# Kernel optimization log

Measured on AMD Instinct MI355X. Metric: run time of the kernel, lower is better.

## Reference

```python
import jax, jax.numpy as jnp
import numpy as np

B, L, E, H = 4, 1024, 1024, 16
D = E // H  # head_dim = 64
K = 3       # conv kernel size
PROB = 0.9  # Bernoulli keep probability


def setup_inputs() -> dict:
    key = jax.random.key(0)
    ks = jax.random.split(key, 8)
    query = jax.random.normal(ks[0], (B, L, E), dtype=jnp.float32)
    keys = jax.random.normal(ks[1], (B, L, E), dtype=jnp.float32)
    values = jax.random.normal(ks[2], (B, L, E), dtype=jnp.float32)
    padding_mask = jax.random.randint(ks[3], (B, L), 0, 2, dtype=jnp.int32)
    causal_mask = jax.random.randint(ks[4], (B, L), 0, 2, dtype=jnp.int32)
    bern_mask = jax.random.bernoulli(ks[5], PROB, (B, H, L)).astype(jnp.int32)
    # learned params: grouped conv (one in/out channel per head) and value linear
    conv_w = jax.random.normal(ks[6], (H, 1, K, K), dtype=jnp.float32) * 0.1
    conv_b = jnp.zeros((H,), dtype=jnp.float32)
    Wv = jax.random.normal(ks[7], (D, D), dtype=jnp.float32) / np.sqrt(D)
    return {"query": query, "keys": keys, "values": values,
            "padding_mask": padding_mask, "causal_mask": causal_mask,
            "bern_mask": bern_mask, "conv_w": conv_w, "conv_b": conv_b, "Wv": Wv}


def _split_heads(x):  # [b, l, (h d)] -> [b, h, l, d]
    b, l, _ = x.shape
    return x.reshape(b, l, H, D).transpose(0, 2, 1, 3)


def reference(query, keys, values, padding_mask, causal_mask, bern_mask, conv_w, conv_b, Wv):
    # queries: grouped conv2d over [b, h=channels, l, d], shape-preserving
    q = _split_heads(query)
    q = jax.lax.conv_general_dilated(
        q, conv_w, window_strides=(1, 1), padding=((1, 1), (1, 1)),
        dimension_numbers=("NCHW", "OIHW", "NCHW"), feature_group_count=H)
    q = q + conv_b[None, :, None, None]
    # keys: Bernoulli-masked fill with -inf, softmax over the SEQ dim (dim=-2)
    k = _split_heads(keys)
    k = jnp.where(bern_mask[..., None].astype(bool), k, -jnp.inf)
    k = jax.nn.softmax(k, axis=-2)
    # values: per-head linear (torch Linear: x @ W^T)
    v = jnp.einsum("bhld,ed->bhle", _split_heads(values), Wv)
    # attention
    energy = jnp.einsum("bhqd,bhkd->bhqk", q, k)
    mask = (padding_mask.astype(bool) & causal_mask.astype(bool))  # [b, k]
    energy = jnp.where(mask[:, None, None, :], jnp.float32(-1e20), energy)
    attn = jax.nn.softmax(energy / jnp.sqrt(jnp.float32(E)), axis=-1)
    out = jnp.einsum("bhqk,bhkd->bhqd", attn, v)
    return out.transpose(0, 2, 1, 3).reshape(query.shape[0], query.shape[1], E)
```

## Files before the change

kernel.cpp:

```cpp
#include <hip/hip_runtime.h>
#include <hip/hip_bf16.h>
#include <math.h>

#define BB 4
#define LL 1024
#define EE 1024
#define HH 16
#define DD 64
#define NCH 8
#define CHROWS 128
#define K2C 0.04508422002777998f
#define BIASC 7.2134752044448f

typedef __attribute__((ext_vector_type(8))) short short8;
typedef __attribute__((ext_vector_type(16))) float f32x16;
typedef __attribute__((ext_vector_type(4))) int int4v;

static __device__ __forceinline__ unsigned short bfbits(float x) {
    __hip_bfloat16 h = __float2bfloat16(x);
    return *(unsigned short*)&h;
}

#define CVTPK(dst, lo_, hi_) \
    asm("v_cvt_pk_bf16_f32 %0, %1, %2" : "=v"(dst) : "v"(lo_), "v"(hi_))
#define PLSWAP(x_, y_) \
    asm("v_permlane32_swap_b32 %0, %1" : "+v"(x_), "+v"(y_))

__global__ __launch_bounds__(256) void prep_kernel(
    const float* __restrict__ query,
    const float* __restrict__ conv_w,
    const float* __restrict__ conv_b,
    const float* __restrict__ values,
    const float* __restrict__ Wv,
    const float* __restrict__ keys,
    const int* __restrict__ bern,
    const int* __restrict__ pad,
    const int* __restrict__ cau,
    __hip_bfloat16* __restrict__ qcb,
    __hip_bfloat16* __restrict__ vt,
    float* __restrict__ pmax,
    float* __restrict__ psum,
    float* __restrict__ maskf) {
    __shared__ __align__(16) char SM[34048];
    int tid = threadIdx.x;
    int bid = blockIdx.x;

    if (bid < 4096) {
        int d = tid & 63;
        int lr = tid >> 6;
        int l0 = (bid & (LL / 4 - 1)) << 2;
        int bh = bid >> 8;
        int h = bh & (HH - 1);
        int b = bh >> 4;
        int l = l0 + lr;

        const float* w = conv_w + h * 9;
        float acc = conv_b[h];
        const float* qin = query + ((size_t)b * LL) * EE + h * DD;
        #pragma unroll
        for (int i = 0; i < 3; ++i) {
            int li = l + i - 1;
            if (li < 0 || li >= LL) continue;
            #pragma unroll
            for (int j = 0; j < 3; ++j) {
                int dj = d + j - 1;
                if (dj < 0 || dj >= DD) continue;
                acc += w[i * 3 + j] * qin[(size_t)li * EE + dj];
            }
        }
        qcb[((size_t)bh * LL + l) * DD + d] = __float2bfloat16(acc);
    } else if (bid < 5120) {
        float (*WvS)[65] = (float(*)[65])SM;
        float (*vs)[68]  = (float(*)[68])(SM + 16640);
        int tile = bid - 4096;
        int lt = tile & 15;
        int bh = tile >> 4;
        int h = bh & (HH - 1);
        int b = bh >> 4;
        int l0 = lt * 64;

        for (int idx = tid; idx < 64 * 64; idx += 256)
            WvS[idx >> 6][idx & 63] = Wv[idx];
        const float* vin = values + ((size_t)b * LL + l0) * EE + h * DD;
        for (int idx = tid; idx < 1024; idx += 256) {
            int r = idx >> 4;
            int c4 = (idx & 15) << 2;
            *(float4*)&vs[r][c4] = *(const float4*)&vin[(size_t)r * EE + c4];
        }
        __syncthreads();

        int d = tid & 63;
        int r0 = (tid >> 6) * 16;
        float acc[16];
        #pragma unroll
        for (int r = 0; r < 16; ++r) acc[r] = 0.f;
        for (int k = 0; k < 64; ++k) {
            float wv = WvS[d][k];
            #pragma unroll
            for (int r = 0; r < 16; ++r) acc[r] += vs[r0 + r][k] * wv;
        }
        union { unsigned short us[16]; uint4 v[2]; } pk;
        #pragma unroll
        for (int r = 0; r < 16; ++r) pk.us[r] = bfbits(acc[r]);
        __hip_bfloat16* vo = vt + ((size_t)bh * DD + d) * LL + l0 + r0;
        *(uint4*)&vo[0] = pk.v[0];
        *(uint4*)&vo[8] = pk.v[1];
    } else {
        float (*sm)[64] = (float(*)[64])SM;
        float (*ss)[64] = (float(*)[64])(SM + 1024);
        int blk = bid - 5120;
        int d = tid & 63;
        int seg = tid >> 6;
        int ch = blk & (NCH - 1);
        int bh = blk >> 3;
        int h = bh & (HH - 1);
        int b = bh >> 4;
        int r0 = ch * CHROWS + seg * 32;

        if (h == 0 && tid < CHROWS) {
            int l = ch * CHROWS + tid;
            maskf[b * LL + l] = ((pad[b * LL + l] != 0) & (cau[b * LL + l] != 0)) ? -1e20f : 0.f;
        }

        const float* kin = keys + ((size_t)b * LL + r0) * EE + h * DD + d;
        const int* bm = bern + (size_t)bh * LL + r0;

        float v[32];
        #pragma unroll
        for (int i = 0; i < 32; ++i) v[i] = kin[(size_t)i * EE];
        float m = -INFINITY;
        #pragma unroll
        for (int i = 0; i < 32; ++i)
            if (bm[i]) m = fmaxf(m, v[i]);
        float s = 0.f;
        #pragma unroll
        for (int i = 0; i < 32; ++i)
            if (bm[i]) s += __expf(v[i] - m);

        sm[seg][d] = m;
        ss[seg][d] = s;
        __syncthreads();
        if (seg == 0) {
            float M = sm[0][d];
            #pragma unroll
            for (int t = 1; t < 4; ++t) M = fmaxf(M, sm[t][d]);
            float S = 0.f;
            if (M > -INFINITY) {
                #pragma unroll
                for (int t = 0; t < 4; ++t)
                    if (sm[t][d] > -INFINITY) S += ss[t][d] * __expf(sm[t][d] - M);
            }
            pmax[(size_t)blk * 64 + d] = M;
            psum[(size_t)blk * 64 + d] = S;
        }
    }
}

__global__ __launch_bounds__(256) void ksm_final_kernel(
    const float* __restrict__ keys,
    const int* __restrict__ bern,
    const float* __restrict__ pmax,
    const float* __restrict__ psum,
    __hip_bfloat16* __restrict__ ksb) {
    int tid = threadIdx.x;
    int d = tid & 63;
    int seg = tid >> 6;
    int blk = blockIdx.x;
    int ch = blk & (NCH - 1);
    int bh = blk >> 3;
    int h = bh & (HH - 1);
    int b = bh >> 4;
    int r0 = ch * CHROWS + seg * 32;

    const float* pm = pmax + (size_t)bh * NCH * 64;
    const float* ps = psum + (size_t)bh * NCH * 64;
    float M = -INFINITY;
    #pragma unroll
    for (int c = 0; c < NCH; ++c) M = fmaxf(M, pm[c * 64 + d]);
    float S = 0.f;
    #pragma unroll
    for (int c = 0; c < NCH; ++c) {
        float mi = pm[c * 64 + d];
        if (mi > -INFINITY) S += ps[c * 64 + d] * __expf(mi - M);
    }
    float inv = 1.f / S;

    const float* kin = keys + ((size_t)b * LL + r0) * EE + h * DD + d;
    const int* bm = bern + (size_t)bh * LL + r0;
    __hip_bfloat16* kout = ksb + ((size_t)bh * LL + r0) * DD + d;
    #pragma unroll
    for (int i = 0; i < 32; ++i) {
        float val = bm[i] ? __expf(kin[(size_t)i * EE] - M) * inv : 0.f;
        kout[(size_t)i * DD] = __float2bfloat16(val);
    }
}

__global__ __launch_bounds__(256) void attn_mfma_kernel(
    const __hip_bfloat16* __restrict__ qcb,
    const __hip_bfloat16* __restrict__ ksb,
    const __hip_bfloat16* __restrict__ vtb,
    const float* __restrict__ maskf,
    float* __restrict__ out) {
    __shared__ __align__(16) short KsS[2][4096];
    __shared__ __align__(16) short VtS[2][4096];
    __shared__ __align__(16) float OutS[4][32 * 36];

    int tid = threadIdx.x;
    int lane = tid & 63;
    int w = tid >> 6;
    int q5 = lane & 31;
    int hi = lane >> 5;

    int bid = blockIdx.x;
    int swz = (bid & 7) * 64 + (bid >> 3);
    int bh = swz >> 3;
    int qb = swz & 7;
    int b = bh >> 4;
    int h = bh & 15;
    int q0w = qb * 128 + w * 32;

    const float* mb = maskf + b * LL;

    int srow = tid >> 3;
    int sch = tid & 7;
    int ssw = (sch ^ (srow & 7)) << 3;
    const __hip_bfloat16* kg = ksb + (size_t)bh * LL * DD + (size_t)srow * DD + ssw;
    const __hip_bfloat16* vg = vtb + (size_t)bh * DD * LL + (size_t)srow * LL + ssw;

    short8 Qf[4];
    {
        const short* qrow = (const short*)qcb + ((size_t)bh * LL + q0w + q5) * DD + 8 * hi;
        #pragma unroll
        for (int i = 0; i < 4; ++i)
            Qf[i] = *(const short8*)(qrow + 16 * i);
    }

    #pragma unroll
    for (int it = 0; it < 2; ++it) {
        __builtin_amdgcn_global_load_lds(
            (const __attribute__((address_space(1))) void*)(kg + (size_t)it * 32 * DD),
            (__attribute__((address_space(3))) void*)&KsS[0][(it * 4 + w) * 512], 16, 0, 0);
        __builtin_amdgcn_global_load_lds(
            (const __attribute__((address_space(1))) void*)(vg + (size_t)it * 32 * LL),
            (__attribute__((address_space(3))) void*)&VtS[0][(it * 4 + w) * 512], 16, 0, 0);
    }
    __syncthreads();

    f32x16 O0, O1;
    #pragma unroll
    for (int e = 0; e < 16; ++e) { O0[e] = 0.f; O1[e] = 0.f; }
    float lrun = 0.f;

    for (int kt = 0; kt < 16; ++kt) {
        int buf = kt & 1;
        int k0 = kt * 64;
        if (kt < 15) {
            int k0n = k0 + 64;
            #pragma unroll
            for (int it = 0; it < 2; ++it) {
                __builtin_amdgcn_global_load_lds(
                    (const __attribute__((address_space(1))) void*)(kg + (size_t)(k0n + it * 32) * DD),
                    (__attribute__((address_space(3))) void*)&KsS[buf ^ 1][(it * 4 + w) * 512], 16, 0, 0);
                __builtin_amdgcn_global_load_lds(
                    (const __attribute__((address_space(1))) void*)(vg + k0n + (size_t)it * 32 * LL),
                    (__attribute__((address_space(3))) void*)&VtS[buf ^ 1][(it * 4 + w) * 512], 16, 0, 0);
            }
        }

        const short* Kb = KsS[buf];
        const short* Vb = VtS[buf];
        int rsw = q5 & 7;

        short8 Ka0[4], Ka1[4], Va0[4], Va1[4];
        #pragma unroll
        for (int i = 0; i < 4; ++i) {
            int off = ((2 * i + hi) ^ rsw) << 3;
            Ka0[i] = *(const short8*)&Kb[q5 * 64 + off];
            Ka1[i] = *(const short8*)&Kb[(32 + q5) * 64 + off];
            Va0[i] = *(const short8*)&Vb[q5 * 64 + off];
            Va1[i] = *(const short8*)&Vb[(32 + q5) * 64 + off];
        }
        float4 mk0[4], mk1[4];
        #pragma unroll
        for (int a = 0; a < 4; ++a) {
            mk0[a] = *(const float4*)&mb[k0 + 8 * a + 4 * hi];
            mk1[a] = *(const float4*)&mb[k0 + 32 + 8 * a + 4 * hi];
        }

        f32x16 S0, S1;
        #pragma unroll
        for (int e = 0; e < 16; ++e) { S0[e] = 0.f; S1[e] = 0.f; }
        __builtin_amdgcn_s_setprio(1);
        #pragma unroll
        for (int i = 0; i < 4; ++i) {
            S0 = __builtin_amdgcn_mfma_f32_32x32x16_bf16(Ka0[i], Qf[i], S0, 0, 0, 0);
            S1 = __builtin_amdgcn_mfma_f32_32x32x16_bf16(Ka1[i], Qf[i], S1, 0, 0, 0);
        }
        __builtin_amdgcn_s_setprio(0);

        float pv[32];
        #pragma unroll
        for (int a = 0; a < 4; ++a) {
            #pragma unroll
            for (int j = 0; j < 4; ++j) {
                float ma0 = __builtin_fmaf(mk0[a][j], K2C, -BIASC);
                float ma1 = __builtin_fmaf(mk1[a][j], K2C, -BIASC);
                pv[4 * a + j]      = exp2f(__builtin_fmaf(S0[4 * a + j], K2C, ma0));
                pv[16 + 4 * a + j] = exp2f(__builtin_fmaf(S1[4 * a + j], K2C, ma1));
            }
        }

        float t16[16];
        #pragma unroll
        for (int r = 0; r < 16; ++r) t16[r] = pv[r] + pv[r + 16];
        float t8[8];
        #pragma unroll
        for (int r = 0; r < 8; ++r) t8[r] = t16[r] + t16[r + 8];
        float rs = ((t8[0] + t8[1]) + (t8[2] + t8[3])) + ((t8[4] + t8[5]) + (t8[6] + t8[7]));
        rs += __shfl_xor(rs, 32, 64);
        lrun += rs;

        union PW { int4v i4; short8 s8; } pa[4];
        #pragma unroll
        for (int st = 0; st < 2; ++st) {
            int c0, d0, c1, d1, c2, d2, c3, d3;
            CVTPK(c0, pv[16 * st + 0], pv[16 * st + 1]);
            CVTPK(d0, pv[16 * st + 4], pv[16 * st + 5]);
            PLSWAP(c0, d0);
            CVTPK(c1, pv[16 * st + 2], pv[16 * st + 3]);
            CVTPK(d1, pv[16 * st + 6], pv[16 * st + 7]);
            PLSWAP(c1, d1);
            pa[2 * st].i4 = (int4v){c0, c1, d0, d1};
            CVTPK(c2, pv[16 * st + 8], pv[16 * st + 9]);
            CVTPK(d2, pv[16 * st + 12], pv[16 * st + 13]);
            PLSWAP(c2, d2);
            CVTPK(c3, pv[16 * st + 10], pv[16 * st + 11]);
            CVTPK(d3, pv[16 * st + 14], pv[16 * st + 15]);
            PLSWAP(c3, d3);
            pa[2 * st + 1].i4 = (int4v){c2, c3, d2, d3};
        }

        __builtin_amdgcn_s_setprio(1);
        #pragma unroll
        for (int ks = 0; ks < 4; ++ks) {
            O0 = __builtin_amdgcn_mfma_f32_32x32x16_bf16(Va0[ks], pa[ks].s8, O0, 0, 0, 0);
            O1 = __builtin_amdgcn_mfma_f32_32x32x16_bf16(Va1[ks], pa[ks].s8, O1, 0, 0, 0);
        }
        __builtin_amdgcn_s_setprio(0);

        if (kt < 15) __syncthreads();
    }

    float invl = 1.f / lrun;
    float* oreg = OutS[w];
    int orow = lane >> 1;
    int ocol = (lane & 1) * 16;

    #pragma unroll
    for (int r = 0; r < 16; ++r) {
        int dl = (r & 3) + 8 * (r >> 2) + 4 * hi;
        oreg[q5 * 36 + dl] = O0[r];
    }
    if (hi == 0) oreg[q5 * 36 + 32] = invl;
    asm volatile("" ::: "memory");
    {
        float iv = oreg[orow * 36 + 32];
        float* gout = out + ((size_t)b * LL + q0w + orow) * EE + h * DD + ocol;
        #pragma unroll
        for (int c = 0; c < 4; ++c) {
            float4 vv = *(float4*)&oreg[orow * 36 + ocol + 4 * c];
            vv.x *= iv; vv.y *= iv; vv.z *= iv; vv.w *= iv;
            *(float4*)&gout[4 * c] = vv;
        }
    }
    asm volatile("" ::: "memory");
    #pragma unroll
    for (int r = 0; r < 16; ++r) {
        int dl = (r & 3) + 8 * (r >> 2) + 4 * hi;
        oreg[q5 * 36 + dl] = O1[r];
    }
    asm volatile("" ::: "memory");
    {
        float iv = oreg[orow * 36 + 32];
        float* gout = out + ((size_t)b * LL + q0w + orow) * EE + h * DD + 32 + ocol;
        #pragma unroll
        for (int c = 0; c < 4; ++c) {
            float4 vv = *(float4*)&oreg[orow * 36 + ocol + 4 * c];
            vv.x *= iv; vv.y *= iv; vv.z *= iv; vv.w *= iv;
            *(float4*)&gout[4 * c] = vv;
        }
    }
}

extern "C" void kernel_launch(void* const* d_in, const int* in_sizes, int n_in,
                              void* d_out, int out_size, void* d_ws, size_t ws_size,
                              hipStream_t stream) {
    const float* query = (const float*)d_in[0];
    const float* keys  = (const float*)d_in[1];
    const float* values = (const float*)d_in[2];
    const int* pad  = (const int*)d_in[3];
    const int* cau  = (const int*)d_in[4];
    const int* bern = (const int*)d_in[5];
    const float* conv_w = (const float*)d_in[6];
    const float* conv_b = (const float*)d_in[7];
    const float* Wv = (const float*)d_in[8];
    float* outp = (float*)d_out;

    const size_t per = (size_t)BB * HH * LL * DD;
    __hip_bfloat16* qcb = (__hip_bfloat16*)d_ws;
    __hip_bfloat16* ksb = qcb + per;
    __hip_bfloat16* vtb = ksb + per;
    float* pmax = (float*)(vtb + per);
    float* psum = pmax + (size_t)BB * HH * NCH * 64;
    float* maskf = psum + (size_t)BB * HH * NCH * 64;

    prep_kernel<<<5632, 256, 0, stream>>>(query, conv_w, conv_b, values, Wv,
                                          keys, bern, pad, cau,
                                          qcb, vtb, pmax, psum, maskf);
    ksm_final_kernel<<<BB * HH * NCH, 256, 0, stream>>>(keys, bern, pmax, psum, ksb);
    attn_mfma_kernel<<<BB * HH * 8, 256, 0, stream>>>(qcb, ksb, vtb, maskf, outp);
}
```

Baseline: 85.68 us.

## Triple-buffer K/V tiles with explicit vmcnt waits and stage mask in LDS

```diff
diff --git a/kernel.cpp b/kernel.cpp
--- a/kernel.cpp
+++ b/kernel.cpp
@@ -201,9 +201,7 @@
     const __hip_bfloat16* __restrict__ vtb,
     const float* __restrict__ maskf,
     float* __restrict__ out) {
-    __shared__ __align__(16) short KsS[2][4096];
-    __shared__ __align__(16) short VtS[2][4096];
-    __shared__ __align__(16) float OutS[4][32 * 36];
+    __shared__ __align__(16) char SMEM[53248];
 
     int tid = threadIdx.x;
     int lane = tid & 63;
@@ -219,13 +217,11 @@
     int h = bh & 15;
     int q0w = qb * 128 + w * 32;
 
-    const float* mb = maskf + b * LL;
-
     int srow = tid >> 3;
     int sch = tid & 7;
     int ssw = (sch ^ (srow & 7)) << 3;
-    const __hip_bfloat16* kg = ksb + (size_t)bh * LL * DD + (size_t)srow * DD + ssw;
-    const __hip_bfloat16* vg = vtb + (size_t)bh * DD * LL + (size_t)srow * LL + ssw;
+    const short* kg = (const short*)ksb + (size_t)bh * LL * DD + (size_t)srow * DD + ssw;
+    const short* vg = (const short*)vtb + (size_t)bh * DD * LL + (size_t)srow * LL + ssw;
 
     short8 Qf[4];
     {
@@ -235,40 +231,53 @@
             Qf[i] = *(const short8*)(qrow + 16 * i);
     }
 
-    #pragma unroll
-    for (int it = 0; it < 2; ++it) {
-        __builtin_amdgcn_global_load_lds(
-            (const __attribute__((address_space(1))) void*)(kg + (size_t)it * 32 * DD),
-            (__attribute__((address_space(3))) void*)&KsS[0][(it * 4 + w) * 512], 16, 0, 0);
-        __builtin_amdgcn_global_load_lds(
-            (const __attribute__((address_space(1))) void*)(vg + (size_t)it * 32 * LL),
-            (__attribute__((address_space(3))) void*)&VtS[0][(it * 4 + w) * 512], 16, 0, 0);
-    }
-    __syncthreads();
+    __builtin_amdgcn_global_load_lds(
+        (const __attribute__((address_space(1))) void*)(maskf + b * LL + tid * 4),
+        (__attribute__((address_space(3))) void*)(SMEM + 49152 + (w * 64) * 16), 16, 0, 0);
+    #pragma unroll
+    for (int t = 0; t < 2; ++t) {
+        #pragma unroll
+        for (int it = 0; it < 2; ++it) {
+            __builtin_amdgcn_global_load_lds(
+                (const __attribute__((address_space(1))) void*)(kg + (size_t)(t * 64 + it * 32) * DD),
+                (__attribute__((address_space(3))) void*)(SMEM + t * 8192 + it * 4096 + w * 1024), 16, 0, 0);
+            __builtin_amdgcn_global_load_lds(
+                (const __attribute__((address_space(1))) void*)(vg + t * 64 + (size_t)it * 32 * LL),
+                (__attribute__((address_space(3))) void*)(SMEM + 24576 + t * 8192 + it * 4096 + w * 1024), 16, 0, 0);
+        }
+    }
 
     f32x16 O0, O1;
     #pragma unroll
     for (int e = 0; e < 16; ++e) { O0[e] = 0.f; O1[e] = 0.f; }
     float lrun = 0.f;
+    const float* mskS = (const float*)(SMEM + 49152);
 
     for (int kt = 0; kt < 16; ++kt) {
-        int buf = kt & 1;
-        int k0 = kt * 64;
         if (kt < 15) {
-            int k0n = k0 + 64;
+            asm volatile("s_waitcnt vmcnt(4)\n\ts_barrier" ::: "memory");
+        } else {
+            asm volatile("s_waitcnt vmcnt(0)\n\ts_barrier" ::: "memory");
+        }
+
+        if (kt <= 13) {
+            int tl = kt + 2;
+            int sl = tl % 3;
             #pragma unroll
             for (int it = 0; it < 2; ++it) {
                 __builtin_amdgcn_global_load_lds(
-                    (const __attribute__((address_space(1))) void*)(kg + (size_t)(k0n + it * 32) * DD),
-                    (__attribute__((address_space(3))) void*)&KsS[buf ^ 1][(it * 4 + w) * 512], 16, 0, 0);
+                    (const __attribute__((address_space(1))) void*)(kg + (size_t)(tl * 64 + it * 32) * DD),
+                    (__attribute__((address_space(3))) void*)(SMEM + sl * 8192 + it * 4096 + w * 1024), 16, 0, 0);
                 __builtin_amdgcn_global_load_lds(
-                    (const __attribute__((address_space(1))) void*)(vg + k0n + (size_t)it * 32 * LL),
-                    (__attribute__((address_space(3))) void*)&VtS[buf ^ 1][(it * 4 + w) * 512], 16, 0, 0);
+                    (const __attribute__((address_space(1))) void*)(vg + tl * 64 + (size_t)it * 32 * LL),
+                    (__attribute__((address_space(3))) void*)(SMEM + 24576 + sl * 8192 + it * 4096 + w * 1024), 16, 0, 0);
             }
         }
 
-        const short* Kb = KsS[buf];
-        const short* Vb = VtS[buf];
+        int slot = kt % 3;
+        int k0 = kt * 64;
+        const short* Kb = (const short*)(SMEM + slot * 8192);
+        const short* Vb = (const short*)(SMEM + 24576 + slot * 8192);
         int rsw = q5 & 7;
 
         short8 Ka0[4], Ka1[4], Va0[4], Va1[4];
@@ -283,8 +292,8 @@
         float4 mk0[4], mk1[4];
         #pragma unroll
         for (int a = 0; a < 4; ++a) {
-            mk0[a] = *(const float4*)&mb[k0 + 8 * a + 4 * hi];
-            mk1[a] = *(const float4*)&mb[k0 + 32 + 8 * a + 4 * hi];
+            mk0[a] = *(const float4*)&mskS[k0 + 8 * a + 4 * hi];
+            mk1[a] = *(const float4*)&mskS[k0 + 32 + 8 * a + 4 * hi];
         }
 
         f32x16 S0, S1;
@@ -302,11 +311,11 @@
         #pragma unroll
         for (int a = 0; a < 4; ++a) {
             #pragma unroll
-            for (int j = 0; j < 4; ++j) {
-                float ma0 = __builtin_fmaf(mk0[a][j], K2C, -BIASC);
-                float ma1 = __builtin_fmaf(mk1[a][j], K2C, -BIASC);
-                pv[4 * a + j]      = exp2f(__builtin_fmaf(S0[4 * a + j], K2C, ma0));
-                pv[16 + 4 * a + j] = exp2f(__builtin_fmaf(S1[4 * a + j], K2C, ma1));
+            for (int jj = 0; jj < 4; ++jj) {
+                float ma0 = __builtin_fmaf(mk0[a][jj], K2C, -BIASC);
+                float ma1 = __builtin_fmaf(mk1[a][jj], K2C, -BIASC);
+                pv[4 * a + jj]      = exp2f(__builtin_fmaf(S0[4 * a + jj], K2C, ma0));
+                pv[16 + 4 * a + jj] = exp2f(__builtin_fmaf(S1[4 * a + jj], K2C, ma1));
             }
         }
 
@@ -347,12 +356,11 @@
             O1 = __builtin_amdgcn_mfma_f32_32x32x16_bf16(Va1[ks], pa[ks].s8, O1, 0, 0, 0);
         }
         __builtin_amdgcn_s_setprio(0);
-
-        if (kt < 15) __syncthreads();
-    }
-
+    }
+
+    __syncthreads();
     float invl = 1.f / lrun;
-    float* oreg = OutS[w];
+    float* oreg = (float*)SMEM + w * (32 * 36);
     int orow = lane >> 1;
     int ocol = (lane & 1) * 16;
 
```

New measurement: 84.13 us. About the same (-1.8%).

## Switch attention to 16x16x32 MFMA tiles with permuted V layout

Applied to the files above, without the earlier changes.

```diff
diff --git a/kernel.cpp b/kernel.cpp
--- a/kernel.cpp
+++ b/kernel.cpp
@@ -13,7 +13,7 @@
 #define BIASC 7.2134752044448f
 
 typedef __attribute__((ext_vector_type(8))) short short8;
-typedef __attribute__((ext_vector_type(16))) float f32x16;
+typedef __attribute__((ext_vector_type(4))) float f32x4;
 typedef __attribute__((ext_vector_type(4))) int int4v;
 
 static __device__ __forceinline__ unsigned short bfbits(float x) {
@@ -23,8 +23,6 @@
 
 #define CVTPK(dst, lo_, hi_) \
     asm("v_cvt_pk_bf16_f32 %0, %1, %2" : "=v"(dst) : "v"(lo_), "v"(hi_))
-#define PLSWAP(x_, y_) \
-    asm("v_permlane32_swap_b32 %0, %1" : "+v"(x_), "+v"(y_))
 
 __global__ __launch_bounds__(256) void prep_kernel(
     const float* __restrict__ query,
@@ -40,7 +38,7 @@
     __hip_bfloat16* __restrict__ vt,
     float* __restrict__ pmax,
     float* __restrict__ psum,
-    float* __restrict__ maskf) {
+    float* __restrict__ mbias) {
     __shared__ __align__(16) char SM[34048];
     int tid = threadIdx.x;
     int bid = blockIdx.x;
@@ -99,12 +97,15 @@
             #pragma unroll
             for (int r = 0; r < 16; ++r) acc[r] += vs[r0 + r][k] * wv;
         }
-        union { unsigned short us[16]; uint4 v[2]; } pk;
+        union { unsigned short us[16]; uint2 u2[4]; } pk;
         #pragma unroll
         for (int r = 0; r < 16; ++r) pk.us[r] = bfbits(acc[r]);
-        __hip_bfloat16* vo = vt + ((size_t)bh * DD + d) * LL + l0 + r0;
-        *(uint4*)&vo[0] = pk.v[0];
-        *(uint4*)&vo[8] = pk.v[1];
+        int C32 = (r0 >> 5) << 5;
+        int h4 = (r0 >> 4) & 1;
+        __hip_bfloat16* vo = vt + ((size_t)bh * DD + d) * LL + l0 + C32 + 4 * h4;
+        #pragma unroll
+        for (int g2 = 0; g2 < 4; ++g2)
+            *(uint2*)&vo[8 * g2] = pk.u2[g2];
     } else {
         float (*sm)[64] = (float(*)[64])SM;
         float (*ss)[64] = (float(*)[64])(SM + 1024);
@@ -119,7 +120,8 @@
 
         if (h == 0 && tid < CHROWS) {
             int l = ch * CHROWS + tid;
-            maskf[b * LL + l] = ((pad[b * LL + l] != 0) & (cau[b * LL + l] != 0)) ? -1e20f : 0.f;
+            int msk = (pad[b * LL + l] != 0) & (cau[b * LL + l] != 0);
+            mbias[b * LL + l] = msk ? (-1e20f * K2C - BIASC) : -BIASC;
         }
 
         const float* kin = keys + ((size_t)b * LL + r0) * EE + h * DD + d;
@@ -199,196 +201,149 @@
     const __hip_bfloat16* __restrict__ qcb,
     const __hip_bfloat16* __restrict__ ksb,
     const __hip_bfloat16* __restrict__ vtb,
-    const float* __restrict__ maskf,
+    const float* __restrict__ mbias,
     float* __restrict__ out) {
     __shared__ __align__(16) short KsS[2][4096];
     __shared__ __align__(16) short VtS[2][4096];
-    __shared__ __align__(16) float OutS[4][32 * 36];
+    __shared__ __align__(16) float mskS[1024];
 
     int tid = threadIdx.x;
     int lane = tid & 63;
     int w = tid >> 6;
-    int q5 = lane & 31;
-    int hi = lane >> 5;
+    int q15 = lane & 15;
+    int g = (lane >> 4) & 3;
 
     int bid = blockIdx.x;
-    int swz = (bid & 7) * 64 + (bid >> 3);
-    int bh = swz >> 3;
-    int qb = swz & 7;
+    int swz = (bid & 7) * 128 + (bid >> 3);
+    int bh = swz >> 4;
+    int qb = swz & 15;
     int b = bh >> 4;
     int h = bh & 15;
-    int q0w = qb * 128 + w * 32;
-
-    const float* mb = maskf + b * LL;
+    int q0w = qb * 64 + w * 16;
 
     int srow = tid >> 3;
     int sch = tid & 7;
     int ssw = (sch ^ (srow & 7)) << 3;
-    const __hip_bfloat16* kg = ksb + (size_t)bh * LL * DD + (size_t)srow * DD + ssw;
-    const __hip_bfloat16* vg = vtb + (size_t)bh * DD * LL + (size_t)srow * LL + ssw;
-
-    short8 Qf[4];
+    const short* kg = (const short*)ksb + (size_t)bh * LL * DD + (size_t)srow * DD + ssw;
+    const short* vg = (const short*)vtb + (size_t)bh * DD * LL + (size_t)srow * LL + ssw;
+
+    short8 Qf0, Qf1;
     {
-        const short* qrow = (const short*)qcb + ((size_t)bh * LL + q0w + q5) * DD + 8 * hi;
-        #pragma unroll
-        for (int i = 0; i < 4; ++i)
-            Qf[i] = *(const short8*)(qrow + 16 * i);
-    }
-
+        const short* qrow = (const short*)qcb + ((size_t)bh * LL + q0w + q15) * DD + 8 * g;
+        Qf0 = *(const short8*)(qrow);
+        Qf1 = *(const short8*)(qrow + 32);
+    }
+
+    __builtin_amdgcn_global_load_lds(
+        (const __attribute__((address_space(1))) void*)(mbias + b * LL + tid * 4),
+        (__attribute__((address_space(3))) void*)&mskS[w * 256], 16, 0, 0);
     #pragma unroll
     for (int it = 0; it < 2; ++it) {
         __builtin_amdgcn_global_load_lds(
-            (const __attribute__((address_space(1))) void*)(kg + (size_t)it * 32 * DD),
+            (const __attribute__((address_space(1))) void*)(kg + (size_t)(it * 32) * DD),
             (__attribute__((address_space(3))) void*)&KsS[0][(it * 4 + w) * 512], 16, 0, 0);
         __builtin_amdgcn_global_load_lds(
             (const __attribute__((address_space(1))) void*)(vg + (size_t)it * 32 * LL),
             (__attribute__((address_space(3))) void*)&VtS[0][(it * 4 + w) * 512], 16, 0, 0);
     }
-    __syncthreads();
-
-    f32x16 O0, O1;
-    #pragma unroll
-    for (int e = 0; e < 16; ++e) { O0[e] = 0.f; O1[e] = 0.f; }
-    float lrun = 0.f;
+
+    f32x4 O[4];
+    #pragma unroll
+    for (int u = 0; u < 4; ++u) O[u] = (f32x4){0.f, 0.f, 0.f, 0.f};
+    float lsum = 0.f;
 
     for (int kt = 0; kt < 16; ++kt) {
-        int buf = kt & 1;
-        int k0 = kt * 64;
+        __syncthreads();
+
         if (kt < 15) {
-            int k0n = k0 + 64;
+            int nb = (kt + 1) & 1;
+            int k0n = (kt + 1) * 64;
             #pragma unroll
             for (int it = 0; it < 2; ++it) {
                 __builtin_amdgcn_global_load_lds(
                     (const __attribute__((address_space(1))) void*)(kg + (size_t)(k0n + it * 32) * DD),
-                    (__attribute__((address_space(3))) void*)&KsS[buf ^ 1][(it * 4 + w) * 512], 16, 0, 0);
+                    (__attribute__((address_space(3))) void*)&KsS[nb][(it * 4 + w) * 512], 16, 0, 0);
                 __builtin_amdgcn_global_load_lds(
                     (const __attribute__((address_space(1))) void*)(vg + k0n + (size_t)it * 32 * LL),
-                    (__attribute__((address_space(3))) void*)&VtS[buf ^ 1][(it * 4 + w) * 512], 16, 0, 0);
+                    (__attribute__((address_space(3))) void*)&VtS[nb][(it * 4 + w) * 512], 16, 0, 0);
             }
         }
 
-        const short* Kb = KsS[buf];
-        const short* Vb = VtS[buf];
-        int rsw = q5 & 7;
-
-        short8 Ka0[4], Ka1[4], Va0[4], Va1[4];
-        #pragma unroll
-        for (int i = 0; i < 4; ++i) {
-            int off = ((2 * i + hi) ^ rsw) << 3;
-            Ka0[i] = *(const short8*)&Kb[q5 * 64 + off];
-            Ka1[i] = *(const short8*)&Kb[(32 + q5) * 64 + off];
-            Va0[i] = *(const short8*)&Vb[q5 * 64 + off];
-            Va1[i] = *(const short8*)&Vb[(32 + q5) * 64 + off];
-        }
-        float4 mk0[4], mk1[4];
-        #pragma unroll
-        for (int a = 0; a < 4; ++a) {
-            mk0[a] = *(const float4*)&mb[k0 + 8 * a + 4 * hi];
-            mk1[a] = *(const float4*)&mb[k0 + 32 + 8 * a + 4 * hi];
-        }
-
-        f32x16 S0, S1;
-        #pragma unroll
-        for (int e = 0; e < 16; ++e) { S0[e] = 0.f; S1[e] = 0.f; }
+        int cb = kt & 1;
+        int k0 = kt * 64;
+        const short* Kb = KsS[cb];
+        const short* Vb = VtS[cb];
+        int sw = q15 & 7;
+        int off0 = (g ^ sw) << 3;
+        int off1 = ((g + 4) ^ sw) << 3;
+
+        f32x4 S[4];
         __builtin_amdgcn_s_setprio(1);
         #pragma unroll
-        for (int i = 0; i < 4; ++i) {
-            S0 = __builtin_amdgcn_mfma_f32_32x32x16_bf16(Ka0[i], Qf[i], S0, 0, 0, 0);
-            S1 = __builtin_amdgcn_mfma_f32_32x32x16_bf16(Ka1[i], Qf[i], S1, 0, 0, 0);
+        for (int t = 0; t < 4; ++t) {
+            short8 kf0 = *(const short8*)&Kb[(16 * t + q15) * 64 + off0];
+            short8 kf1 = *(const short8*)&Kb[(16 * t + q15) * 64 + off1];
+            f32x4 z = (f32x4){0.f, 0.f, 0.f, 0.f};
+            z = __builtin_amdgcn_mfma_f32_16x16x32_bf16(kf0, Qf0, z, 0, 0, 0);
+            S[t] = __builtin_amdgcn_mfma_f32_16x16x32_bf16(kf1, Qf1, z, 0, 0, 0);
         }
         __builtin_amdgcn_s_setprio(0);
 
-        float pv[32];
-        #pragma unroll
-        for (int a = 0; a < 4; ++a) {
-            #pragma unroll
-            for (int j = 0; j < 4; ++j) {
-                float ma0 = __builtin_fmaf(mk0[a][j], K2C, -BIASC);
-                float ma1 = __builtin_fmaf(mk1[a][j], K2C, -BIASC);
-                pv[4 * a + j]      = exp2f(__builtin_fmaf(S0[4 * a + j], K2C, ma0));
-                pv[16 + 4 * a + j] = exp2f(__builtin_fmaf(S1[4 * a + j], K2C, ma1));
-            }
-        }
-
-        float t16[16];
-        #pragma unroll
-        for (int r = 0; r < 16; ++r) t16[r] = pv[r] + pv[r + 16];
-        float t8[8];
-        #pragma unroll
-        for (int r = 0; r < 8; ++r) t8[r] = t16[r] + t16[r + 8];
-        float rs = ((t8[0] + t8[1]) + (t8[2] + t8[3])) + ((t8[4] + t8[5]) + (t8[6] + t8[7]));
-        rs += __shfl_xor(rs, 32, 64);
-        lrun += rs;
-
-        union PW { int4v i4; short8 s8; } pa[4];
-        #pragma unroll
-        for (int st = 0; st < 2; ++st) {
-            int c0, d0, c1, d1, c2, d2, c3, d3;
-            CVTPK(c0, pv[16 * st + 0], pv[16 * st + 1]);
-            CVTPK(d0, pv[16 * st + 4], pv[16 * st + 5]);
-            PLSWAP(c0, d0);
-            CVTPK(c1, pv[16 * st + 2], pv[16 * st + 3]);
-            CVTPK(d1, pv[16 * st + 6], pv[16 * st + 7]);
-            PLSWAP(c1, d1);
-            pa[2 * st].i4 = (int4v){c0, c1, d0, d1};
-            CVTPK(c2, pv[16 * st + 8], pv[16 * st + 9]);
-            CVTPK(d2, pv[16 * st + 12], pv[16 * st + 13]);
-            PLSWAP(c2, d2);
-            CVTPK(c3, pv[16 * st + 10], pv[16 * st + 11]);
-            CVTPK(d3, pv[16 * st + 14], pv[16 * st + 15]);
-            PLSWAP(c3, d3);
-            pa[2 * st + 1].i4 = (int4v){c2, c3, d2, d3};
-        }
+        float4 mb[4];
+        #pragma unroll
+        for (int t = 0; t < 4; ++t)
+            mb[t] = *(const float4*)&mskS[k0 + 16 * t + 4 * g];
+        float pv[4][4];
+        #pragma unroll
+        for (int t = 0; t < 4; ++t)
+            #pragma unroll
+            for (int r = 0; r < 4; ++r)
+                pv[t][r] = exp2f(__builtin_fmaf(S[t][r], K2C, mb[t][r]));
+
+        float s0 = (pv[0][0] + pv[0][1]) + (pv[0][2] + pv[0][3]);
+        float s1 = (pv[1][0] + pv[1][1]) + (pv[1][2] + pv[1][3]);
+        float s2 = (pv[2][0] + pv[2][1]) + (pv[2][2] + pv[2][3]);
+        float s3 = (pv[3][0] + pv[3][1]) + (pv[3][2] + pv[3][3]);
+        lsum += (s0 + s1) + (s2 + s3);
+
+        int4v pa0, pa1;
+        {
+            int d0, d1, d2, d3;
+            CVTPK(d0, pv[0][0], pv[0][1]);
+            CVTPK(d1, pv[0][2], pv[0][3]);
+            CVTPK(d2, pv[1][0], pv[1][1]);
+            CVTPK(d3, pv[1][2], pv[1][3]);
+            pa0 = (int4v){d0, d1, d2, d3};
+            CVTPK(d0, pv[2][0], pv[2][1]);
+            CVTPK(d1, pv[2][2], pv[2][3]);
+            CVTPK(d2, pv[3][0], pv[3][1]);
+            CVTPK(d3, pv[3][2], pv[3][3]);
+            pa1 = (int4v){d0, d1, d2, d3};
+        }
+        union PW { int4v i4; short8 s8; } pw0, pw1;
+        pw0.i4 = pa0;
+        pw1.i4 = pa1;
 
         __builtin_amdgcn_s_setprio(1);
         #pragma unroll
-        for (int ks = 0; ks < 4; ++ks) {
-            O0 = __builtin_amdgcn_mfma_f32_32x32x16_bf16(Va0[ks], pa[ks].s8, O0, 0, 0, 0);
-            O1 = __builtin_amdgcn_mfma_f32_32x32x16_bf16(Va1[ks], pa[ks].s8, O1, 0, 0, 0);
+        for (int u = 0; u < 4; ++u) {
+            short8 vf0 = *(const short8*)&Vb[(16 * u + q15) * 64 + off0];
+            short8 vf1 = *(const short8*)&Vb[(16 * u + q15) * 64 + off1];
+            O[u] = __builtin_amdgcn_mfma_f32_16x16x32_bf16(vf0, pw0.s8, O[u], 0, 0, 0);
+            O[u] = __builtin_amdgcn_mfma_f32_16x16x32_bf16(vf1, pw1.s8, O[u], 0, 0, 0);
         }
         __builtin_amdgcn_s_setprio(0);
-
-        if (kt < 15) __syncthreads();
-    }
-
-    float invl = 1.f / lrun;
-    float* oreg = OutS[w];
-    int orow = lane >> 1;
-    int ocol = (lane & 1) * 16;
-
-    #pragma unroll
-    for (int r = 0; r < 16; ++r) {
-        int dl = (r & 3) + 8 * (r >> 2) + 4 * hi;
-        oreg[q5 * 36 + dl] = O0[r];
-    }
-    if (hi == 0) oreg[q5 * 36 + 32] = invl;
-    asm volatile("" ::: "memory");
-    {
-        float iv = oreg[orow * 36 + 32];
-        float* gout = out + ((size_t)b * LL + q0w + orow) * EE + h * DD + ocol;
-        #pragma unroll
-        for (int c = 0; c < 4; ++c) {
-            float4 vv = *(float4*)&oreg[orow * 36 + ocol + 4 * c];
-            vv.x *= iv; vv.y *= iv; vv.z *= iv; vv.w *= iv;
-            *(float4*)&gout[4 * c] = vv;
-        }
-    }
-    asm volatile("" ::: "memory");
-    #pragma unroll
-    for (int r = 0; r < 16; ++r) {
-        int dl = (r & 3) + 8 * (r >> 2) + 4 * hi;
-        oreg[q5 * 36 + dl] = O1[r];
-    }
-    asm volatile("" ::: "memory");
-    {
-        float iv = oreg[orow * 36 + 32];
-        float* gout = out + ((size_t)b * LL + q0w + orow) * EE + h * DD + 32 + ocol;
-        #pragma unroll
-        for (int c = 0; c < 4; ++c) {
-            float4 vv = *(float4*)&oreg[orow * 36 + ocol + 4 * c];
-            vv.x *= iv; vv.y *= iv; vv.z *= iv; vv.w *= iv;
-            *(float4*)&gout[4 * c] = vv;
-        }
+    }
+
+    lsum += __shfl_xor(lsum, 16, 64);
+    lsum += __shfl_xor(lsum, 32, 64);
+    float invl = 1.f / lsum;
+
+    float* gout = out + ((size_t)b * LL + q0w + q15) * EE + h * DD + 4 * g;
+    #pragma unroll
+    for (int u = 0; u < 4; ++u) {
+        float4 vv = { O[u][0] * invl, O[u][1] * invl, O[u][2] * invl, O[u][3] * invl };
+        *(float4*)&gout[16 * u] = vv;
     }
 }
 
@@ -412,11 +367,11 @@
     __hip_bfloat16* vtb = ksb + per;
     float* pmax = (float*)(vtb + per);
     float* psum = pmax + (size_t)BB * HH * NCH * 64;
-    float* maskf = psum + (size_t)BB * HH * NCH * 64;
+    float* mbias = psum + (size_t)BB * HH * NCH * 64;
 
     prep_kernel<<<5632, 256, 0, stream>>>(query, conv_w, conv_b, values, Wv,
                                           keys, bern, pad, cau,
-                                          qcb, vtb, pmax, psum, maskf);
+                                          qcb, vtb, pmax, psum, mbias);
     ksm_final_kernel<<<BB * HH * NCH, 256, 0, stream>>>(keys, bern, pmax, psum, ksb);
-    attn_mfma_kernel<<<BB * HH * 8, 256, 0, stream>>>(qcb, ksb, vtb, maskf, outp);
-}
+    attn_mfma_kernel<<<BB * HH * 16, 256, 0, stream>>>(qcb, ksb, vtb, mbias, outp);
+}
```

New measurement: 76.86 us. 1.11x faster.
